# Optimization experiments

Measured on AMD Instinct MI355X. Metric: run time of the kernel, lower is better.

The kernel has to match this reference:

```python
import jax, jax.numpy as jnp
import numpy as np

D_MODEL = 2048
N_HEADS = 16
D_HEAD = D_MODEL // N_HEADS
SQLEN = 2048
EPS = 1e-5
XPOS_SCALE_BASE = 512.0


def apply_xpos(x, offset, inv=False):
    # x: (sqlen, d_head). Rotary embedding with xPos exponential length scaling.
    sqlen, d = x.shape
    half = d // 2
    freq = 1.0 / (10000.0 ** (jnp.arange(half, dtype=jnp.float32) / half))
    pos = jnp.arange(sqlen, dtype=jnp.float32) + offset  # absolute positions
    ang = pos[:, None] * freq[None, :]                   # (sqlen, half)
    sin, cos = jnp.sin(ang), jnp.cos(ang)
    # xPos per-dim scale zeta^(pos/scale_base); k gets the inverse scale.
    zeta = (jnp.arange(half, dtype=jnp.float32) * 2.0 + 0.4 * d) / (1.4 * d)
    sc = zeta[None, :] ** (pos[:, None] / XPOS_SCALE_BASE)
    if inv:
        sc = 1.0 / sc
    x1, x2 = x[:, :half], x[:, half:]
    r1 = (x1 * cos - x2 * sin) * sc
    r2 = (x2 * cos + x1 * sin) * sc
    return jnp.concatenate([r1, r2], axis=-1)


def group_norm(x, weight, bias):
    # x: (sqlen, d_model); n_heads groups of d_head channels each.
    xg = x.reshape(x.shape[0], N_HEADS, D_HEAD)
    mu = jnp.mean(xg, axis=-1, keepdims=True)
    var = jnp.mean((xg - mu) ** 2, axis=-1, keepdims=True)
    xn = ((xg - mu) * jax.lax.rsqrt(var + EPS)).reshape(x.shape)
    return xn * weight + bias


def setup_inputs() -> dict:
    key = jax.random.key(0)
    ks = jax.random.split(key, 9)
    s = 0.02
    return {
        "x": jax.random.normal(ks[0], (SQLEN, D_MODEL), dtype=jnp.float32),
        "state": jax.random.normal(ks[1], (N_HEADS, D_HEAD, D_HEAD), dtype=jnp.float32),
        "W_qkv": jax.random.normal(ks[2], (3 * D_MODEL, D_MODEL), dtype=jnp.float32) * s,
        "W_alpha": jax.random.normal(ks[3], (N_HEADS, D_MODEL), dtype=jnp.float32) * s,
        "b_alpha": jnp.zeros((N_HEADS,), dtype=jnp.float32),
        "alpha_base": jnp.log(jax.random.uniform(ks[4], (N_HEADS,), minval=0.95, maxval=0.999)).astype(jnp.float32),
        "gn_weight": jnp.ones((D_MODEL,), dtype=jnp.float32),
        "gn_bias": jnp.zeros((D_MODEL,), dtype=jnp.float32),
        "W_out": jax.random.normal(ks[5], (D_MODEL, D_MODEL), dtype=jnp.float32) * s,
        "W_gate": jax.random.normal(ks[6], (D_MODEL, D_MODEL), dtype=jnp.float32) * s,
        "offset": 0,
    }


def reference(x, state, W_qkv, W_alpha, b_alpha, alpha_base, gn_weight, gn_bias, W_out, W_gate, offset):
    sqlen = x.shape[0]
    # qkv projection -> (3, h, sqlen, d_head)
    qkv = (x @ W_qkv.T).reshape(sqlen, 3, N_HEADS, D_HEAD).transpose(1, 2, 0, 3)
    q, k, v = qkv[0], qkv[1], qkv[2]
    q = jax.vmap(lambda t: apply_xpos(t, offset))(q)
    k = jax.vmap(lambda t: apply_xpos(t, offset, inv=True))(k)

    # per-head, per-position decay log-rates: (h, sqlen), negative
    alphas = jax.nn.sigmoid(x @ W_alpha.T + b_alpha).T
    alphas = alpha_base[:, None] * 8.0 * alphas
    k = (1.0 - jnp.exp(alphas))[:, :, None] * k
    alphas = jnp.cumsum(alphas, axis=1)
    # causal decay matrix Delta[h,i,j] = exp(a_i - a_j) for j <= i
    Delta = jnp.tril(jnp.exp(alphas[:, :, None] - alphas[:, None, :]))

    attn = jnp.einsum('hid,hjd,hij->hij', q, k, Delta)
    ret = jnp.einsum('hij,hje->ihe', attn, v)  # (sqlen, h, d_head)

    # recurrent state carry
    new_state = jnp.exp(alphas[:, -1, None, None]) * state
    ret = ret + jnp.einsum('hid,hde,hi->ihe', q, state, jnp.exp(alphas))
    new_state = new_state + jnp.einsum('hid,hie,hi->hde', k, v, Delta[:, -1, :])

    ret = ret.reshape(sqlen, D_MODEL)
    ret = group_norm(ret, gn_weight, gn_bias)
    out = (jax.nn.swish(ret @ W_gate.T) * ret) @ W_out.T
    return (out, new_state)
```

## Files before the change

kernel.cpp:

```cpp
#include <hip/hip_runtime.h>
#include <cstddef>

#define SQLEN 2048
#define DMODEL 2048
#define NHEADS 16
#define DHEAD 128

typedef __attribute__((ext_vector_type(8))) short bf16x8;
typedef __attribute__((ext_vector_type(4))) float floatx4;

__device__ __forceinline__ unsigned short f2bf(float f) {
  union { float f; unsigned u; } c; c.f = f;
  unsigned u = c.u;
  unsigned r = u + 0x7fffu + ((u >> 16) & 1u);
  return (unsigned short)(r >> 16);
}
__device__ __forceinline__ float bf2f(unsigned short s) {
  union { unsigned u; float f; } c; c.u = ((unsigned)s) << 16;
  return c.f;
}

__global__ __launch_bounds__(256) void f2b_kernel(const float4* __restrict__ in,
                                                  ushort4* __restrict__ out) {
  int i = blockIdx.x * 256 + threadIdx.x;
  float4 v = in[i];
  ushort4 o;
  o.x = f2bf(v.x); o.y = f2bf(v.y); o.z = f2bf(v.z); o.w = f2bf(v.w);
  out[i] = o;
}

__global__ __launch_bounds__(256) void f2b2_kernel(const float4* __restrict__ in0,
                                                   ushort4* __restrict__ out0,
                                                   const float4* __restrict__ in1,
                                                   ushort4* __restrict__ out1,
                                                   int half_blocks) {
  int b = blockIdx.x;
  const float4* in = (b < half_blocks) ? in0 : in1;
  ushort4* out = (b < half_blocks) ? out0 : out1;
  int i = (b < half_blocks ? b : b - half_blocks) * 256 + threadIdx.x;
  float4 v = in[i];
  ushort4 o;
  o.x = f2bf(v.x); o.y = f2bf(v.y); o.z = f2bf(v.z); o.w = f2bf(v.w);
  out[i] = o;
}

__global__ __launch_bounds__(256) void zero_kernel(float4* __restrict__ p) {
  p[blockIdx.x * 256 + threadIdx.x] = (float4){0.f, 0.f, 0.f, 0.f};
}

#define GLD(srcp, dstp) __builtin_amdgcn_global_load_lds( \
    (const __attribute__((address_space(1))) unsigned int*)(srcp), \
    (__attribute__((address_space(3))) unsigned int*)(dstp), 16, 0, 0)

__global__ __launch_bounds__(512, 2) void gemm256_nt(const unsigned short* __restrict__ A,
                                                     const unsigned short* __restrict__ B,
                                                     float* __restrict__ C,
                                                     int M, int N, int K) {
  __shared__ __align__(16) unsigned short lds[65536];
  int tid = threadIdx.x;
  int wave = tid >> 6, lane = tid & 63;
  int wm = wave >> 2, wn = wave & 3;
  int quad = lane >> 4, m16 = lane & 15;
  int sw = m16 & 7;

  int nTN = gridDim.x;
  int lin = blockIdx.y * nTN + blockIdx.x;
  int nwg = gridDim.x * gridDim.y;
  int swzb = (nwg & 7) == 0 ? ((lin & 7) * (nwg >> 3) + (lin >> 3)) : lin;
  int row0 = (swzb / nTN) * 256, col0 = (swzb % nTN) * 256;

  const int nkt = K >> 6;
  const int nit = K >> 7;

  int srow = tid >> 3;
  int scol8 = (((tid & 7) ^ ((tid >> 3) & 7)) * 8);

  bf16x8 a0[2][4], a1[2][4], bb[2][2];
  floatx4 acc[2][2][4][2];
#pragma unroll
  for (int a = 0; a < 2; a++)
#pragma unroll
    for (int b = 0; b < 2; b++)
#pragma unroll
      for (int c = 0; c < 4; c++)
#pragma unroll
        for (int d = 0; d < 2; d++) acc[a][b][c][d] = (floatx4){0.f, 0.f, 0.f, 0.f};

#define STAGE(t_, ab_, h_) do { \
    int t2_ = (t_); if (t2_ >= nkt) t2_ -= nkt; \
    const unsigned short* gp_ = (ab_) ? B : A; \
    int rb_ = ((ab_) ? col0 : row0) + (h_) * 128 + srow; \
    int kk_ = t2_ * 64 + scol8; \
    unsigned bs_ = ((unsigned)((t_) & 1)) * 32768u + (ab_) * 16384u + (h_) * 8192u; \
    GLD(gp_ + (size_t)rb_ * K + kk_, lds + bs_ + tid * 8); \
    GLD(gp_ + (size_t)(rb_ + 64) * K + kk_, lds + bs_ + 4096 + tid * 8); \
  } while (0)

#define VMW asm volatile("s_waitcnt vmcnt(4)" ::: "memory");

#define RDA(dst_, BUF_, MH_) do { \
    const unsigned short* Ab_ = lds + (BUF_) * 32768 + (MH_) * 8192; \
    _Pragma("unroll") for (int ks = 0; ks < 2; ks++) \
      _Pragma("unroll") for (int fi = 0; fi < 4; fi++) \
        dst_[ks][fi] = *(const bf16x8*)(Ab_ + (wm * 64 + fi * 16 + m16) * 64 + (((ks * 4 + quad) ^ sw) * 8)); \
  } while (0)

#define RDB(BUF_, NH_) do { \
    const unsigned short* Bb_ = lds + (BUF_) * 32768 + 16384 + (NH_) * 8192; \
    _Pragma("unroll") for (int ks = 0; ks < 2; ks++) \
      _Pragma("unroll") for (int gj = 0; gj < 2; gj++) \
        bb[ks][gj] = *(const bf16x8*)(Bb_ + (wn * 32 + gj * 16 + m16) * 64 + (((ks * 4 + quad) ^ sw) * 8)); \
  } while (0)

#define MM(A_, MH_, NH_) \
    _Pragma("unroll") for (int ks = 0; ks < 2; ks++) \
      _Pragma("unroll") for (int fi = 0; fi < 4; fi++) \
        _Pragma("unroll") for (int gj = 0; gj < 2; gj++) \
          acc[MH_][NH_][fi][gj] = __builtin_amdgcn_mfma_f32_16x16x32_bf16( \
              A_[ks][fi], bb[ks][gj], acc[MH_][NH_][fi][gj], 0, 0, 0);

#define PH(RD_, STG_, W_, MM_) do { \
    RD_; \
    STG_; \
    W_ \
    __builtin_amdgcn_s_barrier(); \
    asm volatile("s_waitcnt lgkmcnt(0)" ::: "memory"); \
    __builtin_amdgcn_sched_barrier(0); \
    __builtin_amdgcn_s_setprio(1); \
    MM_ \
    __builtin_amdgcn_s_setprio(0); \
    __builtin_amdgcn_sched_barrier(0); \
    __builtin_amdgcn_s_barrier(); \
  } while (0)

  STAGE(0, 1, 0);
  STAGE(0, 0, 0);
  STAGE(0, 0, 1);
  STAGE(0, 1, 1);
  STAGE(1, 1, 0);
  STAGE(1, 0, 0);
  asm volatile("s_waitcnt vmcnt(4)" ::: "memory");
  __builtin_amdgcn_s_barrier();

  for (int it = 0; it < nit; ++it) {
    int T = it * 2;
    PH(RDA(a0, 0, 0); RDB(0, 0), STAGE(T + 1, 0, 1), , MM(a0, 0, 0));
    PH(RDA(a1, 0, 1),            STAGE(T + 1, 1, 1), , MM(a1, 1, 0));
    PH(RDB(0, 1),                STAGE(T + 2, 1, 0), , MM(a0, 0, 1));
    PH(,                         STAGE(T + 2, 0, 0), VMW, MM(a1, 1, 1));
    PH(RDA(a0, 1, 0); RDB(1, 0), STAGE(T + 2, 0, 1), , MM(a0, 0, 0));
    PH(RDA(a1, 1, 1),            STAGE(T + 2, 1, 1), , MM(a1, 1, 0));
    PH(RDB(1, 1),                STAGE(T + 3, 1, 0), , MM(a0, 0, 1));
    PH(,                         STAGE(T + 3, 0, 0), VMW, MM(a1, 1, 1));
  }

#pragma unroll
  for (int mh = 0; mh < 2; mh++)
#pragma unroll
    for (int nh = 0; nh < 2; nh++)
#pragma unroll
      for (int fi = 0; fi < 4; fi++)
#pragma unroll
        for (int gj = 0; gj < 2; gj++) {
          int rr = row0 + mh * 128 + wm * 64 + fi * 16 + quad * 4;
          int cc = col0 + nh * 128 + wn * 32 + gj * 16 + m16;
#pragma unroll
          for (int r = 0; r < 4; r++)
            C[(size_t)(rr + r) * N + cc] = acc[mh][nh][fi][gj][r];
        }
#undef PH
#undef MM
#undef RDB
#undef RDA
#undef VMW
#undef STAGE
}

__global__ __launch_bounds__(256) void gemm_bf16_nt(const unsigned short* __restrict__ A,
                                                    const unsigned short* __restrict__ B,
                                                    float* __restrict__ C,
                                                    int M, int N, int K) {
  __shared__ __align__(16) unsigned short As[128 * 32];
  __shared__ __align__(16) unsigned short Bs[128 * 32];
  int tid = threadIdx.x;
  int wave = tid >> 6;
  int lane = tid & 63;
  int wm = wave >> 1, wn = wave & 1;
  int quad = lane >> 4, m16 = lane & 15;
  int row0 = blockIdx.y * 128, col0 = blockIdx.x * 128;

  floatx4 acc[4][4];
#pragma unroll
  for (int i = 0; i < 4; i++)
#pragma unroll
    for (int j = 0; j < 4; j++) acc[i][j] = (floatx4){0.f, 0.f, 0.f, 0.f};

  int c0 = tid, c1 = tid + 256;
  int r0c = c0 >> 2, q0c = (c0 & 3) * 8;
  int r1c = c1 >> 2, q1c = (c1 & 3) * 8;

  const size_t sK = (size_t)K;
  for (int k0 = 0; k0 < K; k0 += 32) {
    __builtin_amdgcn_global_load_lds(
        (const __attribute__((address_space(1))) unsigned int*)(A + (size_t)(row0 + r0c) * sK + k0 + q0c),
        (__attribute__((address_space(3))) unsigned int*)(As + c0 * 8), 16, 0, 0);
    __builtin_amdgcn_global_load_lds(
        (const __attribute__((address_space(1))) unsigned int*)(A + (size_t)(row0 + r1c) * sK + k0 + q1c),
        (__attribute__((address_space(3))) unsigned int*)(As + c1 * 8), 16, 0, 0);
    __builtin_amdgcn_global_load_lds(
        (const __attribute__((address_space(1))) unsigned int*)(B + (size_t)(col0 + r0c) * sK + k0 + q0c),
        (__attribute__((address_space(3))) unsigned int*)(Bs + c0 * 8), 16, 0, 0);
    __builtin_amdgcn_global_load_lds(
        (const __attribute__((address_space(1))) unsigned int*)(B + (size_t)(col0 + r1c) * sK + k0 + q1c),
        (__attribute__((address_space(3))) unsigned int*)(Bs + c1 * 8), 16, 0, 0);
    __syncthreads();

    bf16x8 af[4], bfr[4];
#pragma unroll
    for (int i = 0; i < 4; i++)
      af[i] = *(const bf16x8*)(As + (wm * 64 + i * 16 + m16) * 32 + quad * 8);
#pragma unroll
    for (int j = 0; j < 4; j++)
      bfr[j] = *(const bf16x8*)(Bs + (wn * 64 + j * 16 + m16) * 32 + quad * 8);
#pragma unroll
    for (int i = 0; i < 4; i++)
#pragma unroll
      for (int j = 0; j < 4; j++)
        acc[i][j] = __builtin_amdgcn_mfma_f32_16x16x32_bf16(af[i], bfr[j], acc[i][j], 0, 0, 0);
    __syncthreads();
  }

#pragma unroll
  for (int i = 0; i < 4; i++) {
#pragma unroll
    for (int j = 0; j < 4; j++) {
      int rr = row0 + wm * 64 + i * 16 + quad * 4;
      int cc = col0 + wn * 64 + j * 16 + m16;
#pragma unroll
      for (int r = 0; r < 4; r++)
        C[(size_t)(rr + r) * N + cc] = acc[i][j][r];
    }
  }
}

__global__ __launch_bounds__(256) void gemm_swish_nt(const unsigned short* __restrict__ A,
                                                     const unsigned short* __restrict__ B,
                                                     const float* __restrict__ rn,
                                                     unsigned short* __restrict__ Hb,
                                                     int M, int N, int K) {
  __shared__ __align__(16) unsigned short As[128 * 32];
  __shared__ __align__(16) unsigned short Bs[128 * 32];
  int tid = threadIdx.x;
  int wave = tid >> 6;
  int lane = tid & 63;
  int wm = wave >> 1, wn = wave & 1;
  int quad = lane >> 4, m16 = lane & 15;
  int row0 = blockIdx.y * 128, col0 = blockIdx.x * 128;

  floatx4 acc[4][4];
#pragma unroll
  for (int i = 0; i < 4; i++)
#pragma unroll
    for (int j = 0; j < 4; j++) acc[i][j] = (floatx4){0.f, 0.f, 0.f, 0.f};

  int c0 = tid, c1 = tid + 256;
  int r0c = c0 >> 2, q0c = (c0 & 3) * 8;
  int r1c = c1 >> 2, q1c = (c1 & 3) * 8;

  const size_t sK = (size_t)K;
  for (int k0 = 0; k0 < K; k0 += 32) {
    __builtin_amdgcn_global_load_lds(
        (const __attribute__((address_space(1))) unsigned int*)(A + (size_t)(row0 + r0c) * sK + k0 + q0c),
        (__attribute__((address_space(3))) unsigned int*)(As + c0 * 8), 16, 0, 0);
    __builtin_amdgcn_global_load_lds(
        (const __attribute__((address_space(1))) unsigned int*)(A + (size_t)(row0 + r1c) * sK + k0 + q1c),
        (__attribute__((address_space(3))) unsigned int*)(As + c1 * 8), 16, 0, 0);
    __builtin_amdgcn_global_load_lds(
        (const __attribute__((address_space(1))) unsigned int*)(B + (size_t)(col0 + r0c) * sK + k0 + q0c),
        (__attribute__((address_space(3))) unsigned int*)(Bs + c0 * 8), 16, 0, 0);
    __builtin_amdgcn_global_load_lds(
        (const __attribute__((address_space(1))) unsigned int*)(B + (size_t)(col0 + r1c) * sK + k0 + q1c),
        (__attribute__((address_space(3))) unsigned int*)(Bs + c1 * 8), 16, 0, 0);
    __syncthreads();

    bf16x8 af[4], bfr[4];
#pragma unroll
    for (int i = 0; i < 4; i++)
      af[i] = *(const bf16x8*)(As + (wm * 64 + i * 16 + m16) * 32 + quad * 8);
#pragma unroll
    for (int j = 0; j < 4; j++)
      bfr[j] = *(const bf16x8*)(Bs + (wn * 64 + j * 16 + m16) * 32 + quad * 8);
#pragma unroll
    for (int i = 0; i < 4; i++)
#pragma unroll
      for (int j = 0; j < 4; j++)
        acc[i][j] = __builtin_amdgcn_mfma_f32_16x16x32_bf16(af[i], bfr[j], acc[i][j], 0, 0, 0);
    __syncthreads();
  }

#pragma unroll
  for (int i = 0; i < 4; i++) {
#pragma unroll
    for (int j = 0; j < 4; j++) {
      int rr = row0 + wm * 64 + i * 16 + quad * 4;
      int cc = col0 + wn * 64 + j * 16 + m16;
#pragma unroll
      for (int r = 0; r < 4; r++) {
        float g = acc[i][j][r];
        float rv = rn[(size_t)(rr + r) * N + cc];
        float hh = g / (1.f + __expf(-g)) * rv;
        Hb[(size_t)(rr + r) * N + cc] = f2bf(hh);
      }
    }
  }
}

__global__ __launch_bounds__(256) void alpha_kernel(const float* __restrict__ x,
                                                    const float* __restrict__ W_alpha,
                                                    const float* __restrict__ b_alpha,
                                                    const float* __restrict__ alpha_base,
                                                    float* __restrict__ a_raw) {
  __shared__ float xs[4][2048];
  int tid = threadIdx.x;
  int t0 = blockIdx.x * 4;
#pragma unroll
  for (int p = 0; p < 8; p++) {
    int idx = tid + p * 256;
    int row = idx >> 9, c4 = idx & 511;
    *(float4*)&xs[row][c4 * 4] = *(const float4*)(x + (size_t)(t0 + row) * DMODEL + c4 * 4);
  }
  __syncthreads();
  int w = tid >> 6, lane = tid & 63;
  int t = t0 + w;
#pragma unroll
  for (int h = 0; h < NHEADS; h++) {
    const float4* wr = (const float4*)(W_alpha + (size_t)h * DMODEL);
    float s = 0.f;
#pragma unroll
    for (int i = lane; i < 512; i += 64) {
      float4 a = *(const float4*)&xs[w][i * 4];
      float4 b = wr[i];
      s += a.x * b.x + a.y * b.y + a.z * b.z + a.w * b.w;
    }
#pragma unroll
    for (int off = 32; off > 0; off >>= 1) s += __shfl_down(s, off);
    if (lane == 0) {
      float sig = 1.f / (1.f + __expf(-(s + b_alpha[h])));
      a_raw[(size_t)h * SQLEN + t] = alpha_base[h] * 8.f * sig;
    }
  }
}

__global__ __launch_bounds__(256) void cumsum_kernel(const float* __restrict__ a_raw,
                                                     float* __restrict__ A) {
  int h = blockIdx.x;
  __shared__ float part[256];
  int tid = threadIdx.x;
  float v[8];
  float s = 0.f;
#pragma unroll
  for (int i = 0; i < 8; i++) {
    v[i] = a_raw[(size_t)h * SQLEN + tid * 8 + i];
    s += v[i];
  }
  part[tid] = s;
  __syncthreads();
  for (int off = 1; off < 256; off <<= 1) {
    float tmp = (tid >= off) ? part[tid - off] : 0.f;
    __syncthreads();
    part[tid] += tmp;
    __syncthreads();
  }
  float run = (tid > 0) ? part[tid - 1] : 0.f;
#pragma unroll
  for (int i = 0; i < 8; i++) {
    run += v[i];
    A[(size_t)h * SQLEN + tid * 8 + i] = run;
  }
}

__global__ __launch_bounds__(256) void xpos_kernel(const float* __restrict__ qkv,
                                                   const float* __restrict__ a_raw,
                                                   const int* __restrict__ offset_p,
                                                   unsigned short* __restrict__ qb,
                                                   unsigned short* __restrict__ kb,
                                                   unsigned short* __restrict__ vb) {
  int idx = blockIdx.x * 256 + threadIdx.x;
  int j = idx & 63;
  int t = (idx >> 6) & 2047;
  int h = idx >> 17;
  float pos = (float)(t + offset_p[0]);
  float freq = exp2f(-(float)j * (13.287712379549449f / 64.f));
  float ang = pos * freq;
  float sn = __sinf(ang), cs = __cosf(ang);
  float zeta = (2.f * (float)j + 51.2f) / 179.2f;
  float lzp = __log2f(zeta) * pos * (1.f / 512.f);
  float sc = exp2f(lzp);
  float sci = exp2f(-lzp);
  const float* row = qkv + (size_t)t * (3 * DMODEL);
  int base = h * DHEAD + j;
  float q1 = row[base], q2 = row[base + 64];
  float k1 = row[DMODEL + base], k2 = row[DMODEL + base + 64];
  float v1 = row[2 * DMODEL + base], v2 = row[2 * DMODEL + base + 64];
  size_t o = ((size_t)h * SQLEN + t) * DHEAD + j;
  qb[o] = f2bf((q1 * cs - q2 * sn) * sc);
  qb[o + 64] = f2bf((q2 * cs + q1 * sn) * sc);
  float km = (1.f - __expf(a_raw[(size_t)h * SQLEN + t])) * sci;
  kb[o] = f2bf((k1 * cs - k2 * sn) * km);
  kb[o + 64] = f2bf((k2 * cs + k1 * sn) * km);
  vb[o] = f2bf(v1);
  vb[o + 64] = f2bf(v2);
}

__global__ __launch_bounds__(256) void transpose_kv_kernel(const unsigned short* __restrict__ kb,
                                                           const unsigned short* __restrict__ vb,
                                                           const float* __restrict__ A,
                                                           unsigned short* __restrict__ kT,
                                                           unsigned short* __restrict__ vT) {
  __shared__ __align__(16) unsigned short tile[64][72];
  int h = blockIdx.z >> 1, sel = blockIdx.z & 1;
  int t0 = blockIdx.x * 64, d0 = blockIdx.y * 64;
  int tid = threadIdx.x;
  const unsigned short* src = (sel ? vb : kb) + ((size_t)h * SQLEN + t0) * DHEAD + d0;
  unsigned short* dst = (sel ? vT : kT) + (size_t)h * (DHEAD * SQLEN) + (size_t)d0 * SQLEN + t0;
  float B = A[(size_t)h * SQLEN + SQLEN - 1];
#pragma unroll
  for (int p = 0; p < 2; p++) {
    int c = tid + p * 256;
    int r = c >> 3, off = (c & 7) * 8;
    bf16x8 in = *(const bf16x8*)(src + (size_t)r * DHEAD + off);
    if (!sel) {
      float w = __expf(B - A[(size_t)h * SQLEN + t0 + r]);
      bf16x8 o;
#pragma unroll
      for (int j = 0; j < 8; j++) o[j] = (short)f2bf(bf2f((unsigned short)in[j]) * w);
      *(bf16x8*)&tile[r][off] = o;
    } else {
      *(bf16x8*)&tile[r][off] = in;
    }
  }
  __syncthreads();
#pragma unroll
  for (int p = 0; p < 2; p++) {
    int c = tid + p * 256;
    int dr = c >> 3, toff = (c & 7) * 8;
    bf16x8 o;
#pragma unroll
    for (int j = 0; j < 8; j++) o[j] = (short)tile[toff + j][dr];
    *(bf16x8*)(dst + (size_t)dr * SQLEN + toff) = o;
  }
}

__global__ __launch_bounds__(256) void transpose_state_kernel(const float* __restrict__ st,
                                                              unsigned short* __restrict__ stT) {
  __shared__ float tile[64][65];
  int h = blockIdx.z, d0 = blockIdx.x * 64, e0 = blockIdx.y * 64;
  int tid = threadIdx.x;
  const float* src = st + (size_t)h * 16384 + (size_t)d0 * DHEAD + e0;
#pragma unroll
  for (int p = 0; p < 4; p++) {
    int idx = tid + p * 256;
    int r = idx >> 4, c = (idx & 15) * 4;
    float4 f = *(const float4*)(src + (size_t)r * DHEAD + c);
    tile[r][c] = f.x; tile[r][c + 1] = f.y; tile[r][c + 2] = f.z; tile[r][c + 3] = f.w;
  }
  __syncthreads();
  unsigned short* dst = stT + (size_t)h * 16384 + (size_t)e0 * DHEAD + d0;
#pragma unroll
  for (int p = 0; p < 2; p++) {
    int idx = tid + p * 256;
    int er = idx >> 3, doff = (idx & 7) * 8;
    bf16x8 o;
#pragma unroll
    for (int j = 0; j < 8; j++) o[j] = (short)f2bf(tile[doff + j][er]);
    *(bf16x8*)(dst + (size_t)er * DHEAD + doff) = o;
  }
}

__global__ __launch_bounds__(256) void retention_partial(const unsigned short* __restrict__ qb,
                                                         const unsigned short* __restrict__ kb,
                                                         const unsigned short* __restrict__ vT,
                                                         const unsigned short* __restrict__ stT,
                                                         const float* __restrict__ A,
                                                         float* __restrict__ R32) {
  __shared__ __align__(16) unsigned short ks[2][64 * 128];
  __shared__ __align__(16) unsigned short vs[2][128 * 64];
  __shared__ __align__(16) unsigned short Ss[64 * 72];
  int h = blockIdx.x;
  int i0 = blockIdx.y * 64;
  int jc = blockIdx.z;
  int jlo = jc * 512;
  if (jlo > i0) return;
  int jhi = min(i0, jlo + 448);
  int tid = threadIdx.x;
  int wave = tid >> 6, lane = tid & 63, quad = lane >> 4, m16 = lane & 15;
  const float* Ah = A + (size_t)h * SQLEN;
  float c = Ah[i0];
  int rq = wave * 16 + m16;

  bool skipl = false;
  if (lane < 32) {
    int j0l = lane * 64;
    if (j0l <= i0) skipl = (c - Ah[j0l + 63] < -87.f);
  }
  unsigned long long smask = __ballot(skipl);
  int j_start = 64 * (int)__builtin_ctzll(~smask);
  int j_begin = max(j_start, jlo);
  bool work = (j_begin <= jhi);
  bool crossw = (jc == 0) && (c > -87.f);
  if (!work && !crossw) return;

  const unsigned short* qh = qb + ((size_t)h * SQLEN + i0 + rq) * DHEAD;
  bf16x8 qf[4];
#pragma unroll
  for (int dc = 0; dc < 4; dc++)
    qf[dc] = *(const bf16x8*)(qh + dc * 32 + quad * 8);
  float ei = __expf(Ah[i0 + rq] - c);

  floatx4 acc[8];
#pragma unroll
  for (int et = 0; et < 8; et++) acc[et] = (floatx4){0.f, 0.f, 0.f, 0.f};

  const unsigned short* khb = kb + (size_t)h * SQLEN * DHEAD;
  const unsigned short* vhb = vT + (size_t)h * (DHEAD * SQLEN);

#define STAGE_KV(b_, j0_) do { \
    const unsigned short* kh_ = khb + (size_t)(j0_) * DHEAD; \
    const unsigned short* vh_ = vhb + (j0_); \
    _Pragma("unroll") for (int p = 0; p < 4; p++) { \
      int cch = tid + p * 256; \
      int r_ = cch >> 4, kp_ = (cch & 15) ^ (r_ & 7); \
      GLD(kh_ + (size_t)r_ * DHEAD + kp_ * 8, &ks[b_][0] + cch * 8); \
      int e_ = cch >> 3, tp_ = (cch & 7) ^ (e_ & 7); \
      GLD(vh_ + (size_t)e_ * SQLEN + tp_ * 8, &vs[b_][0] + cch * 8); \
    } \
  } while (0)

  if (work) STAGE_KV(0, j_begin);

  if (crossw) {
    const unsigned short* sp = stT + (size_t)h * 16384;
    float ecr[4];
#pragma unroll
    for (int r = 0; r < 4; r++) ecr[r] = __expf(Ah[i0 + wave * 16 + quad * 4 + r]);
#pragma unroll
    for (int et = 0; et < 8; et++) {
#pragma unroll
      for (int dc = 0; dc < 4; dc++) {
        bf16x8 sf = *(const bf16x8*)(sp + (et * 16 + m16) * DHEAD + dc * 32 + quad * 8);
        acc[et] = __builtin_amdgcn_mfma_f32_16x16x32_bf16(qf[dc], sf, acc[et], 0, 0, 0);
      }
#pragma unroll
      for (int r = 0; r < 4; r++) acc[et][r] *= ecr[r];
    }
  }

  if (work) {
    int cur = 0;
    for (int j0 = j_begin; j0 <= jhi; j0 += 64) {
      int nxt = j0 + 64;
      float av = Ah[j0 + lane];
      __builtin_amdgcn_sched_barrier(0);
      if (nxt <= jhi) {
        STAGE_KV(cur ^ 1, nxt);
        asm volatile("s_waitcnt vmcnt(8) lgkmcnt(0)" ::: "memory");
      } else {
        asm volatile("s_waitcnt vmcnt(0) lgkmcnt(0)" ::: "memory");
      }
      __builtin_amdgcn_sched_barrier(0);
      asm volatile("s_barrier" ::: "memory");

      float dj = __expf(c - av);

      bool diag = (j0 == i0);
      const unsigned short* ksc = &ks[cur][0];
      const unsigned short* vsc = &vs[cur][0];
#pragma unroll
      for (int jt = 0; jt < 4; jt++) {
        floatx4 s = (floatx4){0.f, 0.f, 0.f, 0.f};
#pragma unroll
        for (int dc = 0; dc < 4; dc++) {
          int rk = jt * 16 + m16;
          bf16x8 kf = *(const bf16x8*)(ksc + rk * 128 + (((dc * 4 + quad) ^ (rk & 7)) * 8));
          s = __builtin_amdgcn_mfma_f32_16x16x32_bf16(kf, qf[dc], s, 0, 0, 0);
        }
        int jb = jt * 16 + quad * 4;
        float d0 = __shfl(dj, jb + 0);
        float d1 = __shfl(dj, jb + 1);
        float d2 = __shfl(dj, jb + 2);
        float d3 = __shfl(dj, jb + 3);
        ushort4 pk;
        pk.x = f2bf((diag && (jb + 0 > rq)) ? 0.f : s[0] * ei * d0);
        pk.y = f2bf((diag && (jb + 1 > rq)) ? 0.f : s[1] * ei * d1);
        pk.z = f2bf((diag && (jb + 2 > rq)) ? 0.f : s[2] * ei * d2);
        pk.w = f2bf((diag && (jb + 3 > rq)) ? 0.f : s[3] * ei * d3);
        *(ushort4*)(Ss + rq * 72 + jb) = pk;
      }

      bf16x8 sfr[2];
#pragma unroll
      for (int kc = 0; kc < 2; kc++)
        sfr[kc] = *(const bf16x8*)(Ss + rq * 72 + kc * 32 + quad * 8);
#pragma unroll
      for (int et = 0; et < 8; et++) {
#pragma unroll
        for (int kc = 0; kc < 2; kc++) {
          int e = et * 16 + m16;
          bf16x8 vf = *(const bf16x8*)(vsc + e * 64 + (((kc * 4 + quad) ^ (e & 7)) * 8));
          acc[et] = __builtin_amdgcn_mfma_f32_16x16x32_bf16(sfr[kc], vf, acc[et], 0, 0, 0);
        }
      }
      asm volatile("s_barrier" ::: "memory");
      cur ^= 1;
    }
  }
#undef STAGE_KV

#pragma unroll
  for (int r = 0; r < 4; r++) {
    int row = i0 + wave * 16 + quad * 4 + r;
    size_t o = (size_t)row * DMODEL + h * DHEAD;
#pragma unroll
    for (int et = 0; et < 8; et++)
      atomicAdd(&R32[o + et * 16 + m16], acc[et][r]);
  }
}

__global__ __launch_bounds__(256) void gn_kernel(const float* __restrict__ R32,
                                                 const float* __restrict__ gn_w,
                                                 const float* __restrict__ gn_b,
                                                 float* __restrict__ rn,
                                                 unsigned short* __restrict__ rnb) {
  int row = blockIdx.x;
  int tid = threadIdx.x;
  const float* src = R32 + (size_t)row * DMODEL + tid * 8;
  float4 a = *(const float4*)src;
  float4 b = *(const float4*)(src + 4);
  float s = a.x + a.y + a.z + a.w + b.x + b.y + b.z + b.w;
  float ss = a.x * a.x + a.y * a.y + a.z * a.z + a.w * a.w +
             b.x * b.x + b.y * b.y + b.z * b.z + b.w * b.w;
#pragma unroll
  for (int off = 8; off > 0; off >>= 1) {
    s += __shfl_xor(s, off);
    ss += __shfl_xor(ss, off);
  }
  float mu = s * (1.f / 128.f);
  float var = ss * (1.f / 128.f) - mu * mu;
  float inv = rsqrtf(var + 1e-5f);
  int col0 = tid * 8;
  const float* wp = gn_w + col0;
  const float* bp = gn_b + col0;
  float v[8] = {a.x, a.y, a.z, a.w, b.x, b.y, b.z, b.w};
  float o[8];
  ushort4 ob[2];
#pragma unroll
  for (int k = 0; k < 8; k++) {
    o[k] = (v[k] - mu) * inv * wp[k] + bp[k];
    ((unsigned short*)ob)[k] = f2bf(o[k]);
  }
  float* rp = rn + (size_t)row * DMODEL + col0;
  *(float4*)rp = (float4){o[0], o[1], o[2], o[3]};
  *(float4*)(rp + 4) = (float4){o[4], o[5], o[6], o[7]};
  *(ushort4*)(rnb + (size_t)row * DMODEL + col0) = ob[0];
  *(ushort4*)(rnb + (size_t)row * DMODEL + col0 + 4) = ob[1];
}

__global__ __launch_bounds__(256) void state_gemm(const unsigned short* __restrict__ kT,
                                                  const unsigned short* __restrict__ vT,
                                                  float* __restrict__ P) {
  __shared__ __align__(16) unsigned short As[128 * 32];
  __shared__ __align__(16) unsigned short Bs[128 * 32];
  int chunk = blockIdx.x, h = blockIdx.y;
  int tid = threadIdx.x;
  int wave = tid >> 6, lane = tid & 63;
  int wm = wave >> 1, wn = wave & 1;
  int quad = lane >> 4, m16 = lane & 15;
  const unsigned short* Ab = kT + (size_t)h * (DHEAD * SQLEN);
  const unsigned short* Bb = vT + (size_t)h * (DHEAD * SQLEN);

  floatx4 acc[4][4];
#pragma unroll
  for (int i = 0; i < 4; i++)
#pragma unroll
    for (int j = 0; j < 4; j++) acc[i][j] = (floatx4){0.f, 0.f, 0.f, 0.f};

  int c0 = tid, c1 = tid + 256;
  int r0c = c0 >> 2, q0c = (c0 & 3) * 8;
  int r1c = c1 >> 2, q1c = (c1 & 3) * 8;

  for (int k0 = chunk * 256; k0 < chunk * 256 + 256; k0 += 32) {
    __builtin_amdgcn_global_load_lds(
        (const __attribute__((address_space(1))) unsigned int*)(Ab + (size_t)r0c * SQLEN + k0 + q0c),
        (__attribute__((address_space(3))) unsigned int*)(As + c0 * 8), 16, 0, 0);
    __builtin_amdgcn_global_load_lds(
        (const __attribute__((address_space(1))) unsigned int*)(Ab + (size_t)r1c * SQLEN + k0 + q1c),
        (__attribute__((address_space(3))) unsigned int*)(As + c1 * 8), 16, 0, 0);
    __builtin_amdgcn_global_load_lds(
        (const __attribute__((address_space(1))) unsigned int*)(Bb + (size_t)r0c * SQLEN + k0 + q0c),
        (__attribute__((address_space(3))) unsigned int*)(Bs + c0 * 8), 16, 0, 0);
    __builtin_amdgcn_global_load_lds(
        (const __attribute__((address_space(1))) unsigned int*)(Bb + (size_t)r1c * SQLEN + k0 + q1c),
        (__attribute__((address_space(3))) unsigned int*)(Bs + c1 * 8), 16, 0, 0);
    __syncthreads();

    bf16x8 af[4], bfr[4];
#pragma unroll
    for (int i = 0; i < 4; i++)
      af[i] = *(const bf16x8*)(As + (wm * 64 + i * 16 + m16) * 32 + quad * 8);
#pragma unroll
    for (int j = 0; j < 4; j++)
      bfr[j] = *(const bf16x8*)(Bs + (wn * 64 + j * 16 + m16) * 32 + quad * 8);
#pragma unroll
    for (int i = 0; i < 4; i++)
#pragma unroll
      for (int j = 0; j < 4; j++)
        acc[i][j] = __builtin_amdgcn_mfma_f32_16x16x32_bf16(af[i], bfr[j], acc[i][j], 0, 0, 0);
    __syncthreads();
  }

  float* Pp = P + (size_t)(h * 8 + chunk) * 16384;
#pragma unroll
  for (int i = 0; i < 4; i++)
#pragma unroll
    for (int j = 0; j < 4; j++) {
      int rr = wm * 64 + i * 16 + quad * 4;
      int cc = wn * 64 + j * 16 + m16;
#pragma unroll
      for (int r = 0; r < 4; r++)
        Pp[(size_t)(rr + r) * DHEAD + cc] = acc[i][j][r];
    }
}

__global__ __launch_bounds__(256) void state_combine(const float* __restrict__ P,
                                                     const float* __restrict__ state,
                                                     const float* __restrict__ A,
                                                     float* __restrict__ out_state) {
  int idx = blockIdx.x * 256 + threadIdx.x;
  int h = idx >> 14;
  int de = idx & 16383;
  float B = A[(size_t)h * SQLEN + SQLEN - 1];
  float s = __expf(B) * state[idx];
#pragma unroll
  for (int c = 0; c < 8; c++) s += P[(size_t)(h * 8 + c) * 16384 + de];
  out_state[idx] = s;
}

extern "C" void kernel_launch(void* const* d_in, const int* in_sizes, int n_in,
                              void* d_out, int out_size, void* d_ws, size_t ws_size,
                              hipStream_t stream) {
  const float* x = (const float*)d_in[0];
  const float* state = (const float*)d_in[1];
  const float* W_qkv = (const float*)d_in[2];
  const float* W_alpha = (const float*)d_in[3];
  const float* b_alpha = (const float*)d_in[4];
  const float* alpha_base = (const float*)d_in[5];
  const float* gn_w = (const float*)d_in[6];
  const float* gn_b = (const float*)d_in[7];
  const float* W_out = (const float*)d_in[8];
  const float* W_gate = (const float*)d_in[9];
  const int* offset = (const int*)d_in[10];

  float* ws = (float*)d_ws;
  float* qkv = ws;
  float* R32 = ws + 4194304;
  float* P   = ws + 8388608;
  float* rn  = ws + 29360128;
  float* araw = ws + 33554432;
  float* Acum = ws + 33587200;

  unsigned short* xb    = (unsigned short*)(ws + 12582912);
  unsigned short* Wqkvb = (unsigned short*)(ws + 16777216);
  unsigned short* qb    = (unsigned short*)(ws + 12582912);
  unsigned short* kb    = (unsigned short*)(ws + 14680064);
  unsigned short* vb    = (unsigned short*)(ws + 16777216);
  unsigned short* kT_s  = (unsigned short*)(ws + 18874368);
  unsigned short* vT_b  = (unsigned short*)(ws + 20971520);
  unsigned short* stT_b = (unsigned short*)(ws + 23068672);
  unsigned short* rnb   = (unsigned short*)(ws + 25165824);
  unsigned short* Wgateb = (unsigned short*)(ws + 14680064);
  unsigned short* Woutb  = (unsigned short*)(ws + 16777216);
  unsigned short* Hb     = (unsigned short*)(ws + 18874368);

  float* out = (float*)d_out;
  float* out_state = out + 4194304;

  dim3 blk(256);
  f2b2_kernel<<<dim3(16384), blk, 0, stream>>>((const float4*)x, (ushort4*)xb,
                                               (const float4*)W_qkv, (ushort4*)Wqkvb, 4096);
  gemm256_nt<<<dim3(24, 8), dim3(512), 0, stream>>>(xb, Wqkvb, qkv, 2048, 6144, 2048);

  alpha_kernel<<<dim3(512), blk, 0, stream>>>(x, W_alpha, b_alpha, alpha_base, araw);
  cumsum_kernel<<<dim3(16), blk, 0, stream>>>(araw, Acum);
  xpos_kernel<<<dim3(8192), blk, 0, stream>>>(qkv, araw, offset, qb, kb, vb);
  zero_kernel<<<dim3(4096), blk, 0, stream>>>((float4*)R32);
  transpose_kv_kernel<<<dim3(32, 2, 32), blk, 0, stream>>>(kb, vb, Acum, kT_s, vT_b);
  transpose_state_kernel<<<dim3(2, 2, 16), blk, 0, stream>>>(state, stT_b);

  retention_partial<<<dim3(16, 32, 4), blk, 0, stream>>>(qb, kb, vT_b, stT_b, Acum, R32);
  gn_kernel<<<dim3(2048), blk, 0, stream>>>(R32, gn_w, gn_b, rn, rnb);

  state_gemm<<<dim3(8, 16), blk, 0, stream>>>(kT_s, vT_b, P);
  state_combine<<<dim3(1024), blk, 0, stream>>>(P, state, Acum, out_state);

  f2b2_kernel<<<dim3(8192), blk, 0, stream>>>((const float4*)W_gate, (ushort4*)Wgateb,
                                              (const float4*)W_out, (ushort4*)Woutb, 4096);
  gemm_swish_nt<<<dim3(16, 16), blk, 0, stream>>>(rnb, Wgateb, rn, Hb, 2048, 2048, 2048);
  gemm_bf16_nt<<<dim3(16, 16), blk, 0, stream>>>(Hb, Woutb, out, 2048, 2048, 2048);
}
```

Baseline: 429.9 us.

## Replace atomic split-K retention accumulation with two-way split and plain stores

The retention kernel now splits the key range into two chunks instead of four and writes each chunk's partial result to its own buffer with plain stores instead of atomicAdd into a zeroed buffer. The group-norm kernel sums the two partial buffers, and the separate zeroing kernel is removed. The P buffer is moved to reuse the qkv region to make room for the second partial buffer. This removes atomic traffic and a launch, but halves the parallelism in the retention grid and lengthens the per-block loop, so load balance across the causal triangle may suffer.

```diff
diff --git a/kernel.cpp b/kernel.cpp
--- a/kernel.cpp
+++ b/kernel.cpp
@@ -42,10 +42,6 @@
   ushort4 o;
   o.x = f2bf(v.x); o.y = f2bf(v.y); o.z = f2bf(v.z); o.w = f2bf(v.w);
   out[i] = o;
-}
-
-__global__ __launch_bounds__(256) void zero_kernel(float4* __restrict__ p) {
-  p[blockIdx.x * 256 + threadIdx.x] = (float4){0.f, 0.f, 0.f, 0.f};
 }
 
 #define GLD(srcp, dstp) __builtin_amdgcn_global_load_lds( \
@@ -477,26 +473,26 @@
   }
 }
 
-__global__ __launch_bounds__(256) void retention_partial(const unsigned short* __restrict__ qb,
-                                                         const unsigned short* __restrict__ kb,
-                                                         const unsigned short* __restrict__ vT,
-                                                         const unsigned short* __restrict__ stT,
-                                                         const float* __restrict__ A,
-                                                         float* __restrict__ R32) {
+__global__ __launch_bounds__(256) void retention_split(const unsigned short* __restrict__ qb,
+                                                       const unsigned short* __restrict__ kb,
+                                                       const unsigned short* __restrict__ vT,
+                                                       const unsigned short* __restrict__ stT,
+                                                       const float* __restrict__ A,
+                                                       float* __restrict__ R32) {
   __shared__ __align__(16) unsigned short ks[2][64 * 128];
   __shared__ __align__(16) unsigned short vs[2][128 * 64];
   __shared__ __align__(16) unsigned short Ss[64 * 72];
   int h = blockIdx.x;
   int i0 = blockIdx.y * 64;
   int jc = blockIdx.z;
-  int jlo = jc * 512;
-  if (jlo > i0) return;
-  int jhi = min(i0, jlo + 448);
+  int jlo = jc * 1024;
+  int jhi = min(i0, jlo + 960);
   int tid = threadIdx.x;
   int wave = tid >> 6, lane = tid & 63, quad = lane >> 4, m16 = lane & 15;
   const float* Ah = A + (size_t)h * SQLEN;
   float c = Ah[i0];
   int rq = wave * 16 + m16;
+  float* Rc = R32 + (size_t)jc * 4194304;
 
   bool skipl = false;
   if (lane < 32) {
@@ -506,23 +502,23 @@
   unsigned long long smask = __ballot(skipl);
   int j_start = 64 * (int)__builtin_ctzll(~smask);
   int j_begin = max(j_start, jlo);
-  bool work = (j_begin <= jhi);
+  bool work = (jlo <= i0) && (j_begin <= jhi);
   bool crossw = (jc == 0) && (c > -87.f);
-  if (!work && !crossw) return;
-
-  const unsigned short* qh = qb + ((size_t)h * SQLEN + i0 + rq) * DHEAD;
-  bf16x8 qf[4];
-#pragma unroll
-  for (int dc = 0; dc < 4; dc++)
-    qf[dc] = *(const bf16x8*)(qh + dc * 32 + quad * 8);
-  float ei = __expf(Ah[i0 + rq] - c);
 
   floatx4 acc[8];
 #pragma unroll
   for (int et = 0; et < 8; et++) acc[et] = (floatx4){0.f, 0.f, 0.f, 0.f};
 
-  const unsigned short* khb = kb + (size_t)h * SQLEN * DHEAD;
-  const unsigned short* vhb = vT + (size_t)h * (DHEAD * SQLEN);
+  if (work || crossw) {
+    const unsigned short* qh = qb + ((size_t)h * SQLEN + i0 + rq) * DHEAD;
+    bf16x8 qf[4];
+#pragma unroll
+    for (int dc = 0; dc < 4; dc++)
+      qf[dc] = *(const bf16x8*)(qh + dc * 32 + quad * 8);
+    float ei = __expf(Ah[i0 + rq] - c);
+
+    const unsigned short* khb = kb + (size_t)h * SQLEN * DHEAD;
+    const unsigned short* vhb = vT + (size_t)h * (DHEAD * SQLEN);
 
 #define STAGE_KV(b_, j0_) do { \
     const unsigned short* kh_ = khb + (size_t)(j0_) * DHEAD; \
@@ -536,85 +532,86 @@
     } \
   } while (0)
 
-  if (work) STAGE_KV(0, j_begin);
-
-  if (crossw) {
-    const unsigned short* sp = stT + (size_t)h * 16384;
-    float ecr[4];
-#pragma unroll
-    for (int r = 0; r < 4; r++) ecr[r] = __expf(Ah[i0 + wave * 16 + quad * 4 + r]);
-#pragma unroll
-    for (int et = 0; et < 8; et++) {
-#pragma unroll
-      for (int dc = 0; dc < 4; dc++) {
-        bf16x8 sf = *(const bf16x8*)(sp + (et * 16 + m16) * DHEAD + dc * 32 + quad * 8);
-        acc[et] = __builtin_amdgcn_mfma_f32_16x16x32_bf16(qf[dc], sf, acc[et], 0, 0, 0);
+    if (work) STAGE_KV(0, j_begin);
+
+    if (crossw) {
+      const unsigned short* sp = stT + (size_t)h * 16384;
+      float ecr[4];
+#pragma unroll
+      for (int r = 0; r < 4; r++) ecr[r] = __expf(Ah[i0 + wave * 16 + quad * 4 + r]);
+#pragma unroll
+      for (int et = 0; et < 8; et++) {
+#pragma unroll
+        for (int dc = 0; dc < 4; dc++) {
+          bf16x8 sf = *(const bf16x8*)(sp + (et * 16 + m16) * DHEAD + dc * 32 + quad * 8);
+          acc[et] = __builtin_amdgcn_mfma_f32_16x16x32_bf16(qf[dc], sf, acc[et], 0, 0, 0);
+        }
+#pragma unroll
+        for (int r = 0; r < 4; r++) acc[et][r] *= ecr[r];
       }
-#pragma unroll
-      for (int r = 0; r < 4; r++) acc[et][r] *= ecr[r];
     }
-  }
-
-  if (work) {
-    int cur = 0;
-    for (int j0 = j_begin; j0 <= jhi; j0 += 64) {
-      int nxt = j0 + 64;
-      float av = Ah[j0 + lane];
-      __builtin_amdgcn_sched_barrier(0);
-      if (nxt <= jhi) {
-        STAGE_KV(cur ^ 1, nxt);
-        asm volatile("s_waitcnt vmcnt(8) lgkmcnt(0)" ::: "memory");
-      } else {
-        asm volatile("s_waitcnt vmcnt(0) lgkmcnt(0)" ::: "memory");
+
+    if (work) {
+      int cur = 0;
+      for (int j0 = j_begin; j0 <= jhi; j0 += 64) {
+        int nxt = j0 + 64;
+        float av = Ah[j0 + lane];
+        __builtin_amdgcn_sched_barrier(0);
+        if (nxt <= jhi) {
+          STAGE_KV(cur ^ 1, nxt);
+          asm volatile("s_waitcnt vmcnt(8) lgkmcnt(0)" ::: "memory");
+        } else {
+          asm volatile("s_waitcnt vmcnt(0) lgkmcnt(0)" ::: "memory");
+        }
+        __builtin_amdgcn_sched_barrier(0);
+        asm volatile("s_barrier" ::: "memory");
+
+        float dj = __expf(c - av);
+
+        bool diag = (j0 == i0);
+        const unsigned short* ksc = &ks[cur][0];
+        const unsigned short* vsc = &vs[cur][0];
+#pragma unroll
+        for (int jt = 0; jt < 4; jt++) {
+          floatx4 s = (floatx4){0.f, 0.f, 0.f, 0.f};
+#pragma unroll
+          for (int dc = 0; dc < 4; dc++) {
+            int rk = jt * 16 + m16;
+            bf16x8 kf = *(const bf16x8*)(ksc + rk * 128 + (((dc * 4 + quad) ^ (rk & 7)) * 8));
+            s = __builtin_amdgcn_mfma_f32_16x16x32_bf16(kf, qf[dc], s, 0, 0, 0);
+          }
+          int jb = jt * 16 + quad * 4;
+          float d0 = __shfl(dj, jb + 0);
+          float d1 = __shfl(dj, jb + 1);
+          float d2 = __shfl(dj, jb + 2);
+          float d3 = __shfl(dj, jb + 3);
+          ushort4 pk;
+          pk.x = f2bf((diag && (jb + 0 > rq)) ? 0.f : s[0] * ei * d0);
+          pk.y = f2bf((diag && (jb + 1 > rq)) ? 0.f : s[1] * ei * d1);
+          pk.z = f2bf((diag && (jb + 2 > rq)) ? 0.f : s[2] * ei * d2);
+          pk.w = f2bf((diag && (jb + 3 > rq)) ? 0.f : s[3] * ei * d3);
+          *(ushort4*)(Ss + rq * 72 + jb) = pk;
+        }
+
+        bf16x8 sfr[2];
+#pragma unroll
+        for (int kc = 0; kc < 2; kc++)
+          sfr[kc] = *(const bf16x8*)(Ss + rq * 72 + kc * 32 + quad * 8);
+#pragma unroll
+        for (int et = 0; et < 8; et++) {
+#pragma unroll
+          for (int kc = 0; kc < 2; kc++) {
+            int e = et * 16 + m16;
+            bf16x8 vf = *(const bf16x8*)(vsc + e * 64 + (((kc * 4 + quad) ^ (e & 7)) * 8));
+            acc[et] = __builtin_amdgcn_mfma_f32_16x16x32_bf16(sfr[kc], vf, acc[et], 0, 0, 0);
+          }
+        }
+        asm volatile("s_barrier" ::: "memory");
+        cur ^= 1;
       }
-      __builtin_amdgcn_sched_barrier(0);
-      asm volatile("s_barrier" ::: "memory");
-
-      float dj = __expf(c - av);
-
-      bool diag = (j0 == i0);
-      const unsigned short* ksc = &ks[cur][0];
-      const unsigned short* vsc = &vs[cur][0];
-#pragma unroll
-      for (int jt = 0; jt < 4; jt++) {
-        floatx4 s = (floatx4){0.f, 0.f, 0.f, 0.f};
-#pragma unroll
-        for (int dc = 0; dc < 4; dc++) {
-          int rk = jt * 16 + m16;
-          bf16x8 kf = *(const bf16x8*)(ksc + rk * 128 + (((dc * 4 + quad) ^ (rk & 7)) * 8));
-          s = __builtin_amdgcn_mfma_f32_16x16x32_bf16(kf, qf[dc], s, 0, 0, 0);
-        }
-        int jb = jt * 16 + quad * 4;
-        float d0 = __shfl(dj, jb + 0);
-        float d1 = __shfl(dj, jb + 1);
-        float d2 = __shfl(dj, jb + 2);
-        float d3 = __shfl(dj, jb + 3);
-        ushort4 pk;
-        pk.x = f2bf((diag && (jb + 0 > rq)) ? 0.f : s[0] * ei * d0);
-        pk.y = f2bf((diag && (jb + 1 > rq)) ? 0.f : s[1] * ei * d1);
-        pk.z = f2bf((diag && (jb + 2 > rq)) ? 0.f : s[2] * ei * d2);
-        pk.w = f2bf((diag && (jb + 3 > rq)) ? 0.f : s[3] * ei * d3);
-        *(ushort4*)(Ss + rq * 72 + jb) = pk;
-      }
-
-      bf16x8 sfr[2];
-#pragma unroll
-      for (int kc = 0; kc < 2; kc++)
-        sfr[kc] = *(const bf16x8*)(Ss + rq * 72 + kc * 32 + quad * 8);
-#pragma unroll
-      for (int et = 0; et < 8; et++) {
-#pragma unroll
-        for (int kc = 0; kc < 2; kc++) {
-          int e = et * 16 + m16;
-          bf16x8 vf = *(const bf16x8*)(vsc + e * 64 + (((kc * 4 + quad) ^ (e & 7)) * 8));
-          acc[et] = __builtin_amdgcn_mfma_f32_16x16x32_bf16(sfr[kc], vf, acc[et], 0, 0, 0);
-        }
-      }
-      asm volatile("s_barrier" ::: "memory");
-      cur ^= 1;
     }
-  }
 #undef STAGE_KV
+  }
 
 #pragma unroll
   for (int r = 0; r < 4; r++) {
@@ -622,7 +619,7 @@
     size_t o = (size_t)row * DMODEL + h * DHEAD;
 #pragma unroll
     for (int et = 0; et < 8; et++)
-      atomicAdd(&R32[o + et * 16 + m16], acc[et][r]);
+      Rc[o + et * 16 + m16] = acc[et][r];
   }
 }
 
@@ -633,12 +630,16 @@
                                                  unsigned short* __restrict__ rnb) {
   int row = blockIdx.x;
   int tid = threadIdx.x;
-  const float* src = R32 + (size_t)row * DMODEL + tid * 8;
-  float4 a = *(const float4*)src;
-  float4 b = *(const float4*)(src + 4);
-  float s = a.x + a.y + a.z + a.w + b.x + b.y + b.z + b.w;
-  float ss = a.x * a.x + a.y * a.y + a.z * a.z + a.w * a.w +
-             b.x * b.x + b.y * b.y + b.z * b.z + b.w * b.w;
+  size_t base = (size_t)row * DMODEL + tid * 8;
+  float4 a0 = *(const float4*)(R32 + base);
+  float4 b0 = *(const float4*)(R32 + base + 4);
+  float4 a1 = *(const float4*)(R32 + 4194304 + base);
+  float4 b1 = *(const float4*)(R32 + 4194304 + base + 4);
+  float v[8] = {a0.x + a1.x, a0.y + a1.y, a0.z + a1.z, a0.w + a1.w,
+                b0.x + b1.x, b0.y + b1.y, b0.z + b1.z, b0.w + b1.w};
+  float s = 0.f, ss = 0.f;
+#pragma unroll
+  for (int k = 0; k < 8; k++) { s += v[k]; ss += v[k] * v[k]; }
 #pragma unroll
   for (int off = 8; off > 0; off >>= 1) {
     s += __shfl_xor(s, off);
@@ -650,7 +651,6 @@
   int col0 = tid * 8;
   const float* wp = gn_w + col0;
   const float* bp = gn_b + col0;
-  float v[8] = {a.x, a.y, a.z, a.w, b.x, b.y, b.z, b.w};
   float o[8];
   ushort4 ob[2];
 #pragma unroll
@@ -762,8 +762,8 @@
 
   float* ws = (float*)d_ws;
   float* qkv = ws;
+  float* P   = ws;
   float* R32 = ws + 4194304;
-  float* P   = ws + 8388608;
   float* rn  = ws + 29360128;
   float* araw = ws + 33554432;
   float* Acum = ws + 33587200;
@@ -792,11 +792,10 @@
   alpha_kernel<<<dim3(512), blk, 0, stream>>>(x, W_alpha, b_alpha, alpha_base, araw);
   cumsum_kernel<<<dim3(16), blk, 0, stream>>>(araw, Acum);
   xpos_kernel<<<dim3(8192), blk, 0, stream>>>(qkv, araw, offset, qb, kb, vb);
-  zero_kernel<<<dim3(4096), blk, 0, stream>>>((float4*)R32);
   transpose_kv_kernel<<<dim3(32, 2, 32), blk, 0, stream>>>(kb, vb, Acum, kT_s, vT_b);
   transpose_state_kernel<<<dim3(2, 2, 16), blk, 0, stream>>>(state, stT_b);
 
-  retention_partial<<<dim3(16, 32, 4), blk, 0, stream>>>(qb, kb, vT_b, stT_b, Acum, R32);
+  retention_split<<<dim3(16, 32, 2), blk, 0, stream>>>(qb, kb, vT_b, stT_b, Acum, R32);
   gn_kernel<<<dim3(2048), blk, 0, stream>>>(R32, gn_w, gn_b, rn, rnb);
 
   state_gemm<<<dim3(8, 16), blk, 0, stream>>>(kT_s, vT_b, P);
```

Measured after the change: 423.4 us. Within noise of the previous version (-1.5%).
